# Kernel tuning notes

Measured on AMD Instinct MI355X. Metric: run time of the kernel, lower is better.

Reference implementation:

```python
import jax, jax.numpy as jnp
import numpy as np

IN, OUT, FP, B, S = 8192, 28672, 128, 32, 1


def setup_inputs() -> dict:
    key = jax.random.key(0)
    k = jax.random.split(key, 6)
    x = jax.random.normal(k[0], (B, S, IN), dtype=jnp.float32).astype(jnp.float16)
    # int8 quantized weight, stored as [OUT, IN]
    weight = jax.random.randint(k[1], (OUT, IN), -128, 128, dtype=jnp.int32).astype(jnp.int8)
    # per-output-column dequant scale (fp16, positive, small)
    scale_col = (jax.random.uniform(k[2], (1, OUT), dtype=jnp.float32) * 0.01 + 1e-4).astype(jnp.float16)
    # fp16 cache of the outlier weight columns [OUT, FP]
    weight_cache = (jax.random.normal(k[3], (OUT, FP), dtype=jnp.float32) * 0.02).astype(jnp.float16)
    bias = (jax.random.normal(k[4], (OUT,), dtype=jnp.float32) * 0.02).astype(jnp.float16)
    # sorted unique outlier column indices
    ind = jnp.sort(jax.random.permutation(k[5], IN)[:FP]).astype(jnp.int32)
    return {"x": x, "weight": weight, "scale_col": scale_col,
            "weight_cache": weight_cache, "bias": bias, "ind": ind}


def reference(x, weight, scale_col, weight_cache, bias, ind):
    out_features = weight.shape[0]
    shape = x.shape[:-1] + (out_features,)
    inputs = x.reshape(-1, x.shape[-1])                       # [M, IN] fp16
    # ExtractOutliersAndSetToZeros: gather outlier activation columns, zero them
    act_outliers = inputs[:, ind]                              # [M, FP] fp16
    tmp = inputs.at[:, ind].set(jnp.float16(0))                # [M, IN]
    # FindRowScale (bit=8): symmetric per-row int8 scale
    x_scale = jnp.max(jnp.abs(tmp), axis=1, keepdims=True) / jnp.float16(127)  # [M, 1]
    q_x = jnp.clip(jnp.round(tmp / x_scale), -128, 127).astype(jnp.int8)       # [M, IN]
    # int8FusedDequantize: int8 GEMM -> dequant with row/col scales -> add fp16 outlier GEMM
    y_int = jnp.matmul(q_x.astype(jnp.int32), weight.T.astype(jnp.int32))      # [M, OUT] int32
    y = y_int.astype(jnp.float16) * x_scale * scale_col                        # dequantize
    y = y + jnp.matmul(act_outliers, weight_cache.T)                           # outlier fp16 GEMM
    y = y + bias
    return y.reshape(shape)
```

## Files before the change

kernel.cpp:

```cpp
#include <hip/hip_runtime.h>
#include <hip/hip_fp16.h>

#define IN_F   8192
#define OUT_F  28672
#define NFP    128
#define NB     32
#define KQTOT  (IN_F / 4)

#define WS_QPK 0
#define WS_XS  262144
#define WS_ACT 263168

typedef int v4i  __attribute__((ext_vector_type(4)));
typedef int v16i __attribute__((ext_vector_type(16)));

__device__ __forceinline__ int pack8(int4 v) {
    return (v.x & 0xFF) | ((v.y & 0xFF) << 8) | ((v.z & 0xFF) << 16) | (v.w << 24);
}

__global__ __launch_bounds__(256) void quant_kernel(
    const float* __restrict__ x, const int* __restrict__ ind,
    int* __restrict__ q_pk, float* __restrict__ xs_out,
    float* __restrict__ act_out)
{
    __shared__ unsigned char flags[IN_F];
    __shared__ float redbuf[4];
    __shared__ float xs_sh;
    const int tid = threadIdx.x;
    const int b = blockIdx.x;

    int* fl4 = (int*)flags;
    for (int i = tid; i < IN_F / 4; i += 256) fl4[i] = 0;
    __syncthreads();
    if (tid < NFP) flags[ind[tid]] = 1;
    __syncthreads();

    const float* xrow = x + (size_t)b * IN_F;
    const float4* x4 = (const float4*)xrow;
    float mx = 0.f;
    for (int c = tid; c < IN_F / 4; c += 256) {
        float4 v = x4[c];
        int fw = fl4[c];
        if (!(fw & 0x000000FF)) mx = fmaxf(mx, fabsf(v.x));
        if (!(fw & 0x0000FF00)) mx = fmaxf(mx, fabsf(v.y));
        if (!(fw & 0x00FF0000)) mx = fmaxf(mx, fabsf(v.z));
        if (!(fw & 0xFF000000)) mx = fmaxf(mx, fabsf(v.w));
    }
    #pragma unroll
    for (int off = 32; off > 0; off >>= 1) {
        float o = __shfl_down(mx, off, 64);
        mx = o > mx ? o : mx;
    }
    if ((tid & 63) == 0) redbuf[tid >> 6] = mx;
    __syncthreads();
    if (tid == 0) {
        float m = redbuf[0];
        #pragma unroll
        for (int i = 1; i < 4; i++) m = redbuf[i] > m ? redbuf[i] : m;
        float xs = __half2float(__float2half_rn(m / 127.0f));
        xs_sh = xs;
        xs_out[b] = xs;
    }
    __syncthreads();
    const float xs = xs_sh;

    for (int c = tid; c < IN_F / 4; c += 256) {
        float4 v = x4[c];
        int fw = fl4[c];
        float ee[4];
        ee[0] = (fw & 0x000000FF) ? 0.f : v.x;
        ee[1] = (fw & 0x0000FF00) ? 0.f : v.y;
        ee[2] = (fw & 0x00FF0000) ? 0.f : v.z;
        ee[3] = (fw & 0xFF000000) ? 0.f : v.w;
        int pk = 0;
        #pragma unroll
        for (int j = 0; j < 4; j++) {
            float qf = __half2float(__float2half_rn(ee[j] / xs));
            float r = rintf(qf);
            r = fminf(fmaxf(r, -128.f), 127.f);
            int qi = (int)r;
            pk |= (qi & 0xFF) << (8 * j);
        }
        q_pk[(size_t)b * KQTOT + c] = pk;
    }
    if (tid < NFP) act_out[b * NFP + tid] = xrow[ind[tid]];
}

#define OT   64
#define KT   256
#define KQT  (KT / 4)
#define WROW 68
#define QROW 68

__global__ __launch_bounds__(128) void gemm_kernel(
    const int* __restrict__ w, const int* __restrict__ q_pk,
    const float* __restrict__ xs_ws, const float* __restrict__ act_ws,
    const float* __restrict__ sc, const float* __restrict__ wc,
    const float* __restrict__ bias, float* __restrict__ out)
{
    __shared__ int   w_p[OT * WROW] __attribute__((aligned(16)));
    __shared__ int   q_t[NB * QROW] __attribute__((aligned(16)));
    __shared__ float act_l[NB * NFP];
    __shared__ float xs_l[NB];

    const int tid  = threadIdx.x;
    const int wave = tid >> 6;
    const int lane = tid & 63;
    const int nl   = lane & 31;
    const int half = lane >> 5;

    const int blk_o = blockIdx.x * OT;
    const int n = blk_o + wave * 32 + nl;

    for (int i = tid; i < NB * NFP; i += 128) act_l[i] = act_ws[i];
    if (tid < NB) xs_l[tid] = xs_ws[tid];

    v16i acc;
    #pragma unroll
    for (int r = 0; r < 16; r++) acc[r] = 0;

    for (int k0 = 0; k0 < IN_F; k0 += KT) {
        __syncthreads();
        #pragma unroll 4
        for (int i = 0; i < 8; i++) {
            int u  = i * 128 + tid;
            int r  = u >> 4;
            int c4 = u & 15;
            const int* src = w + (size_t)(blk_o + r) * IN_F + k0 + c4 * 16;
            int4 a = *(const int4*)(src + 0);
            int4 b = *(const int4*)(src + 4);
            int4 c = *(const int4*)(src + 8);
            int4 d = *(const int4*)(src + 12);
            int4 pk = make_int4(pack8(a), pack8(b), pack8(c), pack8(d));
            *(int4*)&w_p[r * WROW + c4 * 4] = pk;
        }
        #pragma unroll
        for (int i = 0; i < 4; i++) {
            int u  = i * 128 + tid;
            int b  = u >> 4;
            int c4 = u & 15;
            int4 v = *(const int4*)(q_pk + (size_t)b * KQTOT + (k0 >> 2) + c4 * 4);
            *(int4*)&q_t[b * QROW + c4 * 4] = v;
        }
        __syncthreads();

        const int* qrow = &q_t[nl * QROW + half * 4];
        const int* wrow = &w_p[(wave * 32 + nl) * WROW + half * 4];
        #pragma unroll
        for (int s = 0; s < KT / 32; s++) {
            v4i a = *(const v4i*)(qrow + s * 8);
            v4i b = *(const v4i*)(wrow + s * 8);
            acc = __builtin_amdgcn_mfma_i32_32x32x32_i8(a, b, acc, 0, 0, 0);
        }
    }

    const float scn = sc[n];
    const float bin = bias[n];
    const float* wcn = wc + (size_t)n * NFP;

    float dots[16];
    #pragma unroll
    for (int r = 0; r < 16; r++) dots[r] = 0.f;

    for (int j = 0; j < NFP; j += 4) {
        float4 wv = *(const float4*)(wcn + j);
        #pragma unroll
        for (int r = 0; r < 16; r++) {
            int b = (r & 3) + 8 * (r >> 2) + 4 * half;
            float4 av = *(const float4*)(&act_l[b * NFP + j]);
            dots[r] += av.x * wv.x + av.y * wv.y + av.z * wv.z + av.w * wv.w;
        }
    }

    #pragma unroll
    for (int r = 0; r < 16; r++) {
        int b = (r & 3) + 8 * (r >> 2) + 4 * half;
        out[(size_t)b * OUT_F + n] = (float)acc[r] * xs_l[b] * scn + dots[r] + bin;
    }
}

extern "C" void kernel_launch(void* const* d_in, const int* in_sizes, int n_in,
                              void* d_out, int out_size, void* d_ws, size_t ws_size,
                              hipStream_t stream) {
    const float* x    = (const float*)d_in[0];
    const int*   wgt  = (const int*)d_in[1];
    const float* scol = (const float*)d_in[2];
    const float* wch  = (const float*)d_in[3];
    const float* bias = (const float*)d_in[4];
    const int*   ind  = (const int*)d_in[5];
    float* out = (float*)d_out;

    int*   q_pk = (int*)((char*)d_ws + WS_QPK);
    float* xs   = (float*)((char*)d_ws + WS_XS);
    float* act  = (float*)((char*)d_ws + WS_ACT);

    quant_kernel<<<NB, 256, 0, stream>>>(x, ind, q_pk, xs, act);
    gemm_kernel<<<OUT_F / OT, 128, 0, stream>>>(wgt, q_pk, xs, act, scol, wch, bias, out);
}
```

Before: 1.186 ms.

## Split K across four waves with direct register loads and LDS reduction

The GEMM kernel drops the LDS-staged tiles of weights and quantized activations. Each block now covers 32 output columns with four waves, and each wave handles a quarter of K, loading int32-stored weights and packed activations straight from global memory into MFMA operands. Partial accumulators are summed through shared memory, and the outlier dot product is split so each wave computes four batch rows. The aim is to remove the per-tile barriers and LDS traffic and to raise occupancy and the number of blocks (896 instead of 448). The cost is less coalesced, strided per-lane global loads and an extra reduction step.

```diff
diff --git a/kernel.cpp b/kernel.cpp
--- a/kernel.cpp
+++ b/kernel.cpp
@@ -86,96 +86,77 @@
     if (tid < NFP) act_out[b * NFP + tid] = xrow[ind[tid]];
 }
 
-#define OT   64
-#define KT   256
-#define KQT  (KT / 4)
-#define WROW 68
-#define QROW 68
+#define KCHUNK 2048
+#define KSTEPS (KCHUNK / 32)
 
-__global__ __launch_bounds__(128) void gemm_kernel(
+__global__ __launch_bounds__(256, 3) void gemm_kernel(
     const int* __restrict__ w, const int* __restrict__ q_pk,
     const float* __restrict__ xs_ws, const float* __restrict__ act_ws,
     const float* __restrict__ sc, const float* __restrict__ wc,
     const float* __restrict__ bias, float* __restrict__ out)
 {
-    __shared__ int   w_p[OT * WROW] __attribute__((aligned(16)));
-    __shared__ int   q_t[NB * QROW] __attribute__((aligned(16)));
-    __shared__ float act_l[NB * NFP];
-    __shared__ float xs_l[NB];
+    __shared__ int red[4][16][64];
 
     const int tid  = threadIdx.x;
     const int wave = tid >> 6;
     const int lane = tid & 63;
-    const int nl   = lane & 31;
+    const int col  = lane & 31;
     const int half = lane >> 5;
 
-    const int blk_o = blockIdx.x * OT;
-    const int n = blk_o + wave * 32 + nl;
+    const int nb = blockIdx.x * 32;
+    const int n  = nb + col;
 
-    for (int i = tid; i < NB * NFP; i += 128) act_l[i] = act_ws[i];
-    if (tid < NB) xs_l[tid] = xs_ws[tid];
+    const int kbase = wave * KCHUNK;
+    const int* wptr = w    + (size_t)n * IN_F + kbase + half * 16;
+    const int* qptr = q_pk + (size_t)col * KQTOT + (kbase >> 2) + half * 4;
 
     v16i acc;
     #pragma unroll
     for (int r = 0; r < 16; r++) acc[r] = 0;
 
-    for (int k0 = 0; k0 < IN_F; k0 += KT) {
-        __syncthreads();
-        #pragma unroll 4
-        for (int i = 0; i < 8; i++) {
-            int u  = i * 128 + tid;
-            int r  = u >> 4;
-            int c4 = u & 15;
-            const int* src = w + (size_t)(blk_o + r) * IN_F + k0 + c4 * 16;
-            int4 a = *(const int4*)(src + 0);
-            int4 b = *(const int4*)(src + 4);
-            int4 c = *(const int4*)(src + 8);
-            int4 d = *(const int4*)(src + 12);
-            int4 pk = make_int4(pack8(a), pack8(b), pack8(c), pack8(d));
-            *(int4*)&w_p[r * WROW + c4 * 4] = pk;
-        }
-        #pragma unroll
-        for (int i = 0; i < 4; i++) {
-            int u  = i * 128 + tid;
-            int b  = u >> 4;
-            int c4 = u & 15;
-            int4 v = *(const int4*)(q_pk + (size_t)b * KQTOT + (k0 >> 2) + c4 * 4);
-            *(int4*)&q_t[b * QROW + c4 * 4] = v;
-        }
-        __syncthreads();
+    #pragma unroll 4
+    for (int s = 0; s < KSTEPS; s++) {
+        int4 w0 = *(const int4*)(wptr + s * 32 + 0);
+        int4 w1 = *(const int4*)(wptr + s * 32 + 4);
+        int4 w2 = *(const int4*)(wptr + s * 32 + 8);
+        int4 w3 = *(const int4*)(wptr + s * 32 + 12);
+        v4i a = *(const v4i*)(qptr + s * 8);
+        v4i b;
+        b[0] = pack8(w0); b[1] = pack8(w1); b[2] = pack8(w2); b[3] = pack8(w3);
+        acc = __builtin_amdgcn_mfma_i32_32x32x32_i8(a, b, acc, 0, 0, 0);
+    }
 
-        const int* qrow = &q_t[nl * QROW + half * 4];
-        const int* wrow = &w_p[(wave * 32 + nl) * WROW + half * 4];
-        #pragma unroll
-        for (int s = 0; s < KT / 32; s++) {
-            v4i a = *(const v4i*)(qrow + s * 8);
-            v4i b = *(const v4i*)(wrow + s * 8);
-            acc = __builtin_amdgcn_mfma_i32_32x32x32_i8(a, b, acc, 0, 0, 0);
-        }
+    #pragma unroll
+    for (int r = 0; r < 16; r++) red[wave][r][lane] = acc[r];
+    __syncthreads();
+
+    int sum[4];
+    int bidx[4];
+    #pragma unroll
+    for (int j = 0; j < 4; j++) {
+        const int r = wave * 4 + j;
+        sum[j] = red[0][r][lane] + red[1][r][lane] + red[2][r][lane] + red[3][r][lane];
+        bidx[j] = j + 8 * wave + 4 * half;
     }
 
     const float scn = sc[n];
     const float bin = bias[n];
     const float* wcn = wc + (size_t)n * NFP;
 
-    float dots[16];
-    #pragma unroll
-    for (int r = 0; r < 16; r++) dots[r] = 0.f;
-
-    for (int j = 0; j < NFP; j += 4) {
-        float4 wv = *(const float4*)(wcn + j);
+    float dots[4] = {0.f, 0.f, 0.f, 0.f};
+    for (int t = 0; t < NFP; t += 4) {
+        float4 wv4 = *(const float4*)(wcn + t);
         #pragma unroll
-        for (int r = 0; r < 16; r++) {
-            int b = (r & 3) + 8 * (r >> 2) + 4 * half;
-            float4 av = *(const float4*)(&act_l[b * NFP + j]);
-            dots[r] += av.x * wv.x + av.y * wv.y + av.z * wv.z + av.w * wv.w;
+        for (int j = 0; j < 4; j++) {
+            float4 av = *(const float4*)(act_ws + bidx[j] * NFP + t);
+            dots[j] += av.x * wv4.x + av.y * wv4.y + av.z * wv4.z + av.w * wv4.w;
         }
     }
 
     #pragma unroll
-    for (int r = 0; r < 16; r++) {
-        int b = (r & 3) + 8 * (r >> 2) + 4 * half;
-        out[(size_t)b * OUT_F + n] = (float)acc[r] * xs_l[b] * scn + dots[r] + bin;
+    for (int j = 0; j < 4; j++) {
+        const int b = bidx[j];
+        out[(size_t)b * OUT_F + n] = (float)sum[j] * xs_ws[b] * scn + dots[j] + bin;
     }
 }
 
@@ -195,5 +176,5 @@
     float* act  = (float*)((char*)d_ws + WS_ACT);
 
     quant_kernel<<<NB, 256, 0, stream>>>(x, ind, q_pk, xs, act);
-    gemm_kernel<<<OUT_F / OT, 128, 0, stream>>>(wgt, q_pk, xs, act, scol, wch, bias, out);
+    gemm_kernel<<<OUT_F / 32, 256, 0, stream>>>(wgt, q_pk, xs, act, scol, wch, bias, out);
 }
```

Result: slower. 1.277 ms (+7.7%).
